# Kernel tuning notes

Measured on AMD Instinct MI355X. Metric: run time of the kernel, lower is better.

The kernel has to match this reference:

```python
import jax, jax.numpy as jnp
import numpy as np

D = 1024          # d_model
H = 16            # num_attention_heads
HD = D // H       # head_dim
WIN = 512         # attention_window (total)
W = WIN // 2      # one-sided window
S = 4096          # seq_len
B = 2             # batch
NEG = jnp.finfo(jnp.float32).min


def setup_inputs() -> dict:
    key = jax.random.key(0)
    ks = jax.random.split(key, 9)
    sc = 0.02
    return {
        "query": jax.random.normal(ks[0], (S, B, D), dtype=jnp.float32),
        "Wq": jax.random.normal(ks[1], (D, D), dtype=jnp.float32) * sc,
        "bq": jnp.zeros((D,), dtype=jnp.float32),
        "Wk": jax.random.normal(ks[2], (D, D), dtype=jnp.float32) * sc,
        "bk": jnp.zeros((D,), dtype=jnp.float32),
        "Wv": jax.random.normal(ks[3], (D, D), dtype=jnp.float32) * sc,
        "bv": jnp.zeros((D,), dtype=jnp.float32),
        "Wo": jax.random.normal(ks[4], (D, D), dtype=jnp.float32) * sc,
        "bo": jnp.zeros((D,), dtype=jnp.float32),
    }


def _heads(x):  # [B,S,D] -> [B,H,S,HD]
    b, s, _ = x.shape
    return x.reshape(b, s, H, HD).transpose(0, 2, 1, 3)


def reference(query, Wq, bq, Wk, bk, Wv, bv, Wo, bo):
    s, b, d = query.shape
    x = query.transpose(1, 0, 2)                       # [B,S,D]
    q = _heads(x @ Wq + bq) / jnp.sqrt(jnp.float32(HD))  # [B,H,S,HD]
    k = _heads(x @ Wk + bk)
    v = _heads(x @ Wv + bv)

    nc = s // W                                        # number of chunks
    # pad keys/values with one window of zeros on each side of seq axis
    kp = jnp.pad(k, ((0, 0), (0, 0), (W, W), (0, 0)))  # [B,H,S+2W,HD]
    vp = jnp.pad(v, ((0, 0), (0, 0), (W, W), (0, 0)))
    idx = jnp.arange(nc)[:, None] * W + jnp.arange(3 * W)[None, :]  # [nc,3W]
    kc = kp[:, :, idx]                                 # [B,H,nc,3W,HD]
    vc = vp[:, :, idx]
    qc = q.reshape(b, H, nc, W, HD)                    # [B,H,nc,W,HD]

    scores = jnp.einsum("bhcrd,bhckd->bhcrk", qc, kc)  # [B,H,nc,W,3W]

    r = jnp.arange(W)[:, None]                         # query offset in chunk
    kk = jnp.arange(3 * W)[None, :]
    band = (kk >= r) & (kk <= r + 2 * W)               # |kpos-qpos| <= W
    kpos = jnp.arange(nc)[:, None, None] * W + kk[None] - W   # [nc,1,3W] global key pos
    mask = band[None] & (kpos >= 0) & (kpos < s)       # [nc,W,3W]

    scores = jnp.where(mask[None, None], scores, NEG)
    probs = jax.nn.softmax(scores, axis=-1)
    out = jnp.einsum("bhcrk,bhckd->bhcrd", probs, vc)  # [B,H,nc,W,HD]
    out = out.reshape(b, H, s, HD).transpose(0, 2, 1, 3).reshape(b, s, d)
    out = out.transpose(1, 0, 2)                       # [S,B,D]
    return out @ Wo + bo
```

## Files before the change

kernel.cpp:

```cpp
#include <hip/hip_runtime.h>
#include <hip/hip_bf16.h>

#define SEQ 4096
#define BATCH 2
#define DMODEL 1024
#define NH 16
#define HDIM 64
#define NEGM (-1.0e30f)
#define NT 16

typedef __attribute__((ext_vector_type(8))) short bf16x8;
typedef __attribute__((ext_vector_type(8))) unsigned short us8;
typedef __attribute__((ext_vector_type(4))) unsigned short us4;
typedef __attribute__((ext_vector_type(4))) float f32x4;

__device__ __forceinline__ unsigned short f2bf(float f) {
    union { float f; unsigned u; } v; v.f = f;
    unsigned u = v.u;
    return (unsigned short)((u + 0x7fffu + ((u >> 16) & 1u)) >> 16);
}

#define GL16(g, l)                                                              \
    __builtin_amdgcn_global_load_lds(                                           \
        (const __attribute__((address_space(1))) unsigned int*)(g),             \
        (__attribute__((address_space(3))) unsigned int*)(l), 16, 0, 0)

__global__ __launch_bounds__(256) void transpose_all(const float* __restrict__ Wq,
                                                     const float* __restrict__ Wk,
                                                     const float* __restrict__ Wv,
                                                     const float* __restrict__ Wo,
                                                     unsigned short* __restrict__ wcat,
                                                     unsigned short* __restrict__ wot) {
    const int z = blockIdx.z;
    const float* W = (z == 0) ? Wq : (z == 1) ? Wk : (z == 2) ? Wv : Wo;
    unsigned short* Wt = (z == 3) ? wot : wcat + (size_t)z * 1024 * 1024;
    const float scale = (z == 0) ? 0.125f : 1.0f;
    __shared__ float tile[64][65];
    const int n0 = blockIdx.x * 64, k0 = blockIdx.y * 64;
    const int tx = threadIdx.x;
    for (int dy = threadIdx.y; dy < 64; dy += 4)
        tile[dy][tx] = W[(size_t)(k0 + dy) * DMODEL + n0 + tx];
    __syncthreads();
    for (int dy = threadIdx.y; dy < 64; dy += 4)
        Wt[(size_t)(n0 + dy) * DMODEL + k0 + tx] = f2bf(tile[tx][dy] * scale);
}

__global__ __launch_bounds__(256) void convert_x_bcat(const float* __restrict__ q,
                                                      unsigned short* __restrict__ xb,
                                                      const float* __restrict__ bq,
                                                      const float* __restrict__ bk,
                                                      const float* __restrict__ bv,
                                                      float* __restrict__ bcat) {
    const int bid = blockIdx.x;
    if (bid >= 8192) {
        int i = (bid - 8192) * 256 + threadIdx.x;
        float v;
        if (i < 1024) v = bq[i] * 0.125f;
        else if (i < 2048) v = bk[i - 1024];
        else v = bv[i - 2048];
        bcat[i] = v;
        return;
    }
    int t = bid * 256 + threadIdx.x;
    int d4 = (t & 255) * 4;
    int row = t >> 8;
    int b = row >> 12, s = row & (SEQ - 1);
    float4 v = *(const float4*)(q + ((size_t)s * BATCH + b) * DMODEL + d4);
    us4 o;
    o[0] = f2bf(v.x); o[1] = f2bf(v.y); o[2] = f2bf(v.z); o[3] = f2bf(v.w);
    *(us4*)(xb + (size_t)row * DMODEL + d4) = o;
}

__device__ __forceinline__ void store_qkv(float v0, float v1, float v2, float v3,
                                          int row0, int col, float bval,
                                          unsigned short* __restrict__ qb,
                                          unsigned short* __restrict__ kb,
                                          unsigned short* __restrict__ vtb) {
    const int proj = col >> 10;
    const int ch = col & 1023;
    const int h = ch >> 6, hd = ch & 63;
    float vv[4] = {v0, v1, v2, v3};
    if (proj == 2) {
        const int b = row0 >> 12, s = row0 & (SEQ - 1);
        us4 o;
#pragma unroll
        for (int r = 0; r < 4; ++r) o[r] = f2bf(vv[r] + bval);
        *(us4*)(vtb + ((size_t)(b * NH + h) * HDIM + hd) * SEQ + s) = o;
    } else {
        unsigned short* dst = (proj == 0) ? qb : kb;
#pragma unroll
        for (int r = 0; r < 4; ++r) {
            const int row = row0 + r;
            const int b = row >> 12, s = row & (SEQ - 1);
            dst[((size_t)(b * NH + h) * SEQ + s) * HDIM + hd] = f2bf(vv[r] + bval);
        }
    }
}

__global__ __launch_bounds__(512) void gemm192(const unsigned short* __restrict__ A,
                                               const unsigned short* __restrict__ Bt,
                                               const float* __restrict__ bias,
                                               unsigned short* __restrict__ qb,
                                               unsigned short* __restrict__ kb,
                                               unsigned short* __restrict__ vtb) {
    __shared__ __align__(16) unsigned short lds[57344];
    const int tid = threadIdx.x;
    const int lane = tid & 63, wid = tid >> 6;
    const int lr = lane & 15, lg = lane >> 4;
    const int wm = wid >> 2, wn = wid & 3;
    const int cpx = (int)gridDim.x >> 3;
    const int orig = ((int)blockIdx.x & 7) * cpx + ((int)blockIdx.x >> 3);
    const int m0 = (orig >> 4) * 256;
    const int n0 = (orig & 15) * 192;

    const int srow = wid * 8 + (lane >> 3);
    const int scol = ((lane & 7) ^ (lane >> 3)) << 3;

    f32x4 acc[8][3];
#pragma unroll
    for (int m = 0; m < 8; ++m)
#pragma unroll
        for (int n = 0; n < 3; ++n) {
            f32x4 z = {0.f, 0.f, 0.f, 0.f};
            acc[m][n] = z;
        }

    const unsigned short* gA = A + (size_t)(m0 + srow) * DMODEL + scol;
    const unsigned short* gB = Bt + (size_t)(n0 + srow) * DMODEL + scol;

#define STAGE192(kt, bsel)                                                       \
    do {                                                                         \
        const unsigned short* ga_ = gA + (kt) * 64;                              \
        unsigned short* la_ = &lds[(bsel) * 28672 + wid * 512];                  \
        _Pragma("unroll")                                                        \
        for (int r_ = 0; r_ < 4; ++r_)                                           \
            GL16(ga_ + (size_t)r_ * 64 * DMODEL, la_ + r_ * 4096);               \
        const unsigned short* gb_ = gB + (kt) * 64;                              \
        unsigned short* lb_ = &lds[(bsel) * 28672 + 16384 + wid * 512];          \
        _Pragma("unroll")                                                        \
        for (int r_ = 0; r_ < 3; ++r_)                                           \
            GL16(gb_ + (size_t)r_ * 64 * DMODEL, lb_ + r_ * 4096);               \
    } while (0)

    STAGE192(0, 0);
    asm volatile("s_waitcnt vmcnt(0)" ::: "memory");
    __builtin_amdgcn_s_barrier();
    asm volatile("" ::: "memory");

    const int swz = (lr & 7) << 3;
    for (int t = 0; t < NT; ++t) {
        if (t + 1 < NT) STAGE192(t + 1, (t + 1) & 1);
        const unsigned short* Ab = &lds[(t & 1) * 28672];
        const unsigned short* Bb = Ab + 16384;
#pragma unroll
        for (int ks = 0; ks < 2; ++ks) {
            const int kc = (ks * 32 + lg * 8) ^ swz;
            bf16x8 af[8], bfr[3];
#pragma unroll
            for (int fm = 0; fm < 8; ++fm)
                af[fm] = *(const bf16x8*)&Ab[(wm * 128 + fm * 16 + lr) * 64 + kc];
#pragma unroll
            for (int fn = 0; fn < 3; ++fn)
                bfr[fn] = *(const bf16x8*)&Bb[(wn * 48 + fn * 16 + lr) * 64 + kc];
            __builtin_amdgcn_s_setprio(1);
#pragma unroll
            for (int fm = 0; fm < 8; ++fm)
#pragma unroll
                for (int fn = 0; fn < 3; ++fn)
                    acc[fm][fn] = __builtin_amdgcn_mfma_f32_16x16x32_bf16(af[fm], bfr[fn], acc[fm][fn], 0, 0, 0);
            __builtin_amdgcn_s_setprio(0);
        }
        __builtin_amdgcn_sched_barrier(0);
        asm volatile("s_waitcnt lgkmcnt(0)" ::: "memory");
        asm volatile("s_waitcnt vmcnt(0)" ::: "memory");
        __builtin_amdgcn_s_barrier();
        asm volatile("" ::: "memory");
    }
#undef STAGE192

#pragma unroll
    for (int fn = 0; fn < 3; ++fn) {
        const int col = n0 + wn * 48 + fn * 16 + lr;
        const float bval = bias[col];
#pragma unroll
        for (int fm = 0; fm < 8; ++fm) {
            const int row0 = m0 + wm * 128 + fm * 16 + lg * 4;
            store_qkv(acc[fm][fn][0], acc[fm][fn][1], acc[fm][fn][2], acc[fm][fn][3],
                      row0, col, bval, qb, kb, vtb);
        }
    }
}

__global__ __launch_bounds__(512) void gemm256o(const unsigned short* __restrict__ A,
                                                const unsigned short* __restrict__ Bt,
                                                const float* __restrict__ bias,
                                                float* __restrict__ out) {
    __shared__ __align__(16) unsigned short lds[73728];
    const int tid = threadIdx.x;
    const int lane = tid & 63, wid = tid >> 6;
    const int lr = lane & 15, lg = lane >> 4;
    const int wm = wid >> 1, wn = wid & 1;
    const int cpx = (int)gridDim.x >> 3;
    const int orig = ((int)blockIdx.x & 7) * cpx + ((int)blockIdx.x >> 3);
    const int m0 = (orig >> 3) * 256;
    const int n0 = (orig & 7) * 128;

    const int srow = wid * 8 + (lane >> 3);
    const int scol = ((lane & 7) ^ (lane >> 3)) << 3;

    f32x4 acc[4][4];
#pragma unroll
    for (int m = 0; m < 4; ++m)
#pragma unroll
        for (int n = 0; n < 4; ++n) {
            f32x4 z = {0.f, 0.f, 0.f, 0.f};
            acc[m][n] = z;
        }

    const unsigned short* gA = A + (size_t)(m0 + srow) * DMODEL + scol;
    const unsigned short* gB = Bt + (size_t)(n0 + srow) * DMODEL + scol;

#define STAGE_A(kt, bsel)                                                        \
    do {                                                                         \
        const unsigned short* ga_ = gA + (kt) * 64;                              \
        unsigned short* la_ = &lds[(bsel) * 24576 + wid * 512];                  \
        _Pragma("unroll")                                                        \
        for (int r_ = 0; r_ < 4; ++r_)                                           \
            GL16(ga_ + (size_t)r_ * 64 * DMODEL, la_ + r_ * 4096);               \
    } while (0)
#define STAGE_B(kt, bsel)                                                        \
    do {                                                                         \
        const unsigned short* gb_ = gB + (kt) * 64;                              \
        unsigned short* lb_ = &lds[(bsel) * 24576 + 16384 + wid * 512];          \
        _Pragma("unroll")                                                        \
        for (int r_ = 0; r_ < 2; ++r_)                                           \
            GL16(gb_ + (size_t)r_ * 64 * DMODEL, lb_ + r_ * 4096);               \
    } while (0)

    STAGE_A(0, 0); STAGE_B(0, 0);
    STAGE_A(1, 1); STAGE_B(1, 1);
    asm volatile("s_waitcnt vmcnt(6)" ::: "memory");
    __builtin_amdgcn_s_barrier();
    asm volatile("" ::: "memory");

    const int swz = (lr & 7) << 3;
    int bs = 0;
    for (int t = 0; t < NT; ++t) {
        const int b2 = bs >= 1 ? bs - 1 : bs + 2;
        if (t + 2 < NT) { STAGE_A(t + 2, b2); STAGE_B(t + 2, b2); }
        const unsigned short* Ab = &lds[bs * 24576];
        const unsigned short* Bb = Ab + 16384;
#pragma unroll
        for (int ks = 0; ks < 2; ++ks) {
            const int kc = (ks * 32 + lg * 8) ^ swz;
            bf16x8 af[4], bfr[4];
#pragma unroll
            for (int fm = 0; fm < 4; ++fm)
                af[fm] = *(const bf16x8*)&Ab[(wm * 64 + fm * 16 + lr) * 64 + kc];
#pragma unroll
            for (int fn = 0; fn < 4; ++fn)
                bfr[fn] = *(const bf16x8*)&Bb[(wn * 64 + fn * 16 + lr) * 64 + kc];
            __builtin_amdgcn_s_setprio(1);
#pragma unroll
            for (int fm = 0; fm < 4; ++fm)
#pragma unroll
                for (int fn = 0; fn < 4; ++fn)
                    acc[fm][fn] = __builtin_amdgcn_mfma_f32_16x16x32_bf16(af[fm], bfr[fn], acc[fm][fn], 0, 0, 0);
            __builtin_amdgcn_s_setprio(0);
        }
        __builtin_amdgcn_sched_barrier(0);
        asm volatile("s_waitcnt lgkmcnt(0)" ::: "memory");
        if (t + 2 < NT)
            asm volatile("s_waitcnt vmcnt(6)" ::: "memory");
        else
            asm volatile("s_waitcnt vmcnt(0)" ::: "memory");
        __builtin_amdgcn_s_barrier();
        asm volatile("" ::: "memory");
        bs = bs < 2 ? bs + 1 : 0;
    }
#undef STAGE_A
#undef STAGE_B

#pragma unroll
    for (int fn = 0; fn < 4; ++fn) {
        const int col = n0 + wn * 64 + fn * 16 + lr;
        const float bval = bias[col];
#pragma unroll
        for (int fm = 0; fm < 4; ++fm) {
            const int row0 = m0 + wm * 64 + fm * 16 + lg * 4;
#pragma unroll
            for (int r = 0; r < 4; ++r) {
                const int row = row0 + r;
                const int b = row >> 12, s = row & (SEQ - 1);
                out[((size_t)s * BATCH + b) * DMODEL + col] = acc[fm][fn][r] + bval;
            }
        }
    }
}

__global__ __launch_bounds__(512) void attn_kernel(const unsigned short* __restrict__ qb,
                                                   const unsigned short* __restrict__ kb,
                                                   const unsigned short* __restrict__ vtb,
                                                   unsigned short* __restrict__ ao) {
    __shared__ __align__(16) unsigned short Ks[64][72];
    __shared__ __align__(16) unsigned short Vs[64][72];
    __shared__ __align__(16) unsigned short Ps[8][16][72];
    const int tid = threadIdx.x;
    const int lane = tid & 63, wid = tid >> 6;
    const int lr = lane & 15, lg = lane >> 4;
    const int blk = ((int)blockIdx.x & 7) * 128 + ((int)blockIdx.x >> 3);
    const int qc = blk & 31, h = (blk >> 5) & 15, b = blk >> 9;
    const int q0 = qc * 128;
    const unsigned short* Qh = qb + (size_t)(b * NH + h) * SEQ * HDIM;
    const unsigned short* Kh = kb + (size_t)(b * NH + h) * SEQ * HDIM;
    const unsigned short* Vh = vtb + (size_t)(b * NH + h) * HDIM * SEQ;
    const int qw = q0 + wid * 16;

    bf16x8 qf0 = *(const bf16x8*)(Qh + (size_t)(qw + lr) * HDIM + lg * 8);
    bf16x8 qf1 = *(const bf16x8*)(Qh + (size_t)(qw + lr) * HDIM + 32 + lg * 8);

    f32x4 oacc[4];
    float lsum[4];
#pragma unroll
    for (int n = 0; n < 4; ++n) {
        f32x4 z = {0.f, 0.f, 0.f, 0.f};
        oacc[n] = z;
    }
#pragma unroll
    for (int r = 0; r < 4; ++r) lsum[r] = 0.f;

    int lo = q0 - 256; if (lo < 0) lo = 0;
    int hi = q0 + 384; if (hi > SEQ) hi = SEQ;

    const int srow = tid >> 3, sseg = (tid & 7) * 8;

    us8 kpre = *(const us8*)(Kh + (size_t)(lo + srow) * HDIM + sseg);
    us8 vpre = *(const us8*)(Vh + (size_t)srow * SEQ + lo + sseg);

    for (int kt = lo; kt < hi; kt += 64) {
        __syncthreads();
        *(us8*)&Ks[srow][sseg] = kpre;
        *(us8*)&Vs[srow][sseg] = vpre;
        if (kt + 64 < hi) {
            kpre = *(const us8*)(Kh + (size_t)(kt + 64 + srow) * HDIM + sseg);
            vpre = *(const us8*)(Vh + (size_t)srow * SEQ + kt + 64 + sseg);
        }
        __builtin_amdgcn_sched_barrier(0);
        __syncthreads();

        f32x4 sf[4];
        __builtin_amdgcn_s_setprio(1);
#pragma unroll
        for (int n = 0; n < 4; ++n) {
            bf16x8 kf0 = *(const bf16x8*)&Ks[n * 16 + lr][lg * 8];
            bf16x8 kf1 = *(const bf16x8*)&Ks[n * 16 + lr][32 + lg * 8];
            f32x4 z = {0.f, 0.f, 0.f, 0.f};
            sf[n] = __builtin_amdgcn_mfma_f32_16x16x32_bf16(qf0, kf0, z, 0, 0, 0);
            sf[n] = __builtin_amdgcn_mfma_f32_16x16x32_bf16(qf1, kf1, sf[n], 0, 0, 0);
        }
        __builtin_amdgcn_s_setprio(0);
        const bool full = (kt >= qw - 241) && (kt + 63 <= qw + 256);
        if (!full) {
#pragma unroll
            for (int r = 0; r < 4; ++r) {
                const int qpos = qw + lg * 4 + r;
#pragma unroll
                for (int n = 0; n < 4; ++n) {
                    const int kpos = kt + n * 16 + lr;
                    if (kpos < qpos - 256 || kpos > qpos + 256) sf[n][r] = NEGM;
                }
            }
        }
#pragma unroll
        for (int n = 0; n < 4; ++n)
#pragma unroll
            for (int r = 0; r < 4; ++r) {
                const float p = __expf(sf[n][r]);
                lsum[r] += p;
                Ps[wid][lg * 4 + r][n * 16 + lr] = f2bf(p);
            }

        asm volatile("s_waitcnt lgkmcnt(0)" ::: "memory");
        __builtin_amdgcn_s_setprio(1);
#pragma unroll
        for (int ks = 0; ks < 2; ++ks) {
            bf16x8 pf = *(const bf16x8*)&Ps[wid][lr][ks * 32 + lg * 8];
#pragma unroll
            for (int n = 0; n < 4; ++n) {
                bf16x8 vf = *(const bf16x8*)&Vs[n * 16 + lr][ks * 32 + lg * 8];
                oacc[n] = __builtin_amdgcn_mfma_f32_16x16x32_bf16(pf, vf, oacc[n], 0, 0, 0);
            }
        }
        __builtin_amdgcn_s_setprio(0);
    }

#pragma unroll
    for (int d = 1; d < 16; d <<= 1)
#pragma unroll
        for (int r = 0; r < 4; ++r) lsum[r] += __shfl_xor(lsum[r], d, 64);

#pragma unroll
    for (int n = 0; n < 4; ++n)
#pragma unroll
        for (int r = 0; r < 4; ++r) {
            const int row = qw + lg * 4 + r;
            const float o = oacc[n][r] / lsum[r];
            ao[((size_t)b * SEQ + row) * DMODEL + h * HDIM + n * 16 + lr] = f2bf(o);
        }
}

extern "C" void kernel_launch(void* const* d_in, const int* in_sizes, int n_in,
                              void* d_out, int out_size, void* d_ws, size_t ws_size,
                              hipStream_t stream) {
    (void)in_sizes; (void)n_in; (void)out_size; (void)ws_size;
    const float* query = (const float*)d_in[0];
    const float* Wq = (const float*)d_in[1];
    const float* bq = (const float*)d_in[2];
    const float* Wk = (const float*)d_in[3];
    const float* bk = (const float*)d_in[4];
    const float* Wv = (const float*)d_in[5];
    const float* bv = (const float*)d_in[6];
    const float* Wo = (const float*)d_in[7];
    const float* bo = (const float*)d_in[8];
    float* out = (float*)d_out;

    char* ws = (char*)d_ws;
    unsigned short* xb   = (unsigned short*)ws;
    unsigned short* wcat = (unsigned short*)(ws + (16ull << 20));
    unsigned short* wot  = (unsigned short*)(ws + (22ull << 20));
    float*          bcat = (float*)(ws + (24ull << 20));
    unsigned short* qb   = (unsigned short*)(ws + (25ull << 20));
    unsigned short* kb   = (unsigned short*)(ws + (41ull << 20));
    unsigned short* vtb  = (unsigned short*)(ws + (57ull << 20));
    unsigned short* ao   = xb;

    transpose_all<<<dim3(16, 16, 4), dim3(64, 4), 0, stream>>>(Wq, Wk, Wv, Wo, wcat, wot);
    convert_x_bcat<<<8204, 256, 0, stream>>>(query, xb, bq, bk, bv, bcat);

    gemm192<<<512, 512, 0, stream>>>(xb, wcat, bcat, qb, kb, vtb);
    attn_kernel<<<1024, 512, 0, stream>>>(qb, kb, vtb, ao);
    gemm256o<<<256, 512, 0, stream>>>(ao, wot, bo, out);
}
```

Before: 149.0 us.

## Merge prep kernels, reshape QKV warp tiling, shrink output GEMM tiles

Fuses the weight transpose and the input/bias conversion into one launch, which saves a kernel launch. The QKV GEMM's 8 waves are regrouped from a 2x4 grid of 128x48 tiles to a 4x2 grid of 64x96 tiles, which changes the LDS fragment loads per MFMA. The output projection now uses 128x128 tiles with 256 threads and a single LDS buffer, so more blocks fit per CU for occupancy. In exchange it drops the triple-buffered load pipelining, so global loads no longer overlap with the MFMA work.

```diff
diff --git a/kernel.cpp b/kernel.cpp
--- a/kernel.cpp
+++ b/kernel.cpp
@@ -25,50 +25,50 @@
         (const __attribute__((address_space(1))) unsigned int*)(g),             \
         (__attribute__((address_space(3))) unsigned int*)(l), 16, 0, 0)
 
-__global__ __launch_bounds__(256) void transpose_all(const float* __restrict__ Wq,
-                                                     const float* __restrict__ Wk,
-                                                     const float* __restrict__ Wv,
-                                                     const float* __restrict__ Wo,
-                                                     unsigned short* __restrict__ wcat,
-                                                     unsigned short* __restrict__ wot) {
-    const int z = blockIdx.z;
-    const float* W = (z == 0) ? Wq : (z == 1) ? Wk : (z == 2) ? Wv : Wo;
-    unsigned short* Wt = (z == 3) ? wot : wcat + (size_t)z * 1024 * 1024;
-    const float scale = (z == 0) ? 0.125f : 1.0f;
+__global__ __launch_bounds__(256) void prep_all(const float* __restrict__ Wq,
+                                                const float* __restrict__ Wk,
+                                                const float* __restrict__ Wv,
+                                                const float* __restrict__ Wo,
+                                                const float* __restrict__ query,
+                                                const float* __restrict__ bq,
+                                                const float* __restrict__ bk,
+                                                const float* __restrict__ bv,
+                                                unsigned short* __restrict__ wcat,
+                                                unsigned short* __restrict__ wot,
+                                                unsigned short* __restrict__ xb,
+                                                float* __restrict__ bcat) {
     __shared__ float tile[64][65];
-    const int n0 = blockIdx.x * 64, k0 = blockIdx.y * 64;
-    const int tx = threadIdx.x;
-    for (int dy = threadIdx.y; dy < 64; dy += 4)
-        tile[dy][tx] = W[(size_t)(k0 + dy) * DMODEL + n0 + tx];
-    __syncthreads();
-    for (int dy = threadIdx.y; dy < 64; dy += 4)
-        Wt[(size_t)(n0 + dy) * DMODEL + k0 + tx] = f2bf(tile[tx][dy] * scale);
-}
-
-__global__ __launch_bounds__(256) void convert_x_bcat(const float* __restrict__ q,
-                                                      unsigned short* __restrict__ xb,
-                                                      const float* __restrict__ bq,
-                                                      const float* __restrict__ bk,
-                                                      const float* __restrict__ bv,
-                                                      float* __restrict__ bcat) {
     const int bid = blockIdx.x;
-    if (bid >= 8192) {
-        int i = (bid - 8192) * 256 + threadIdx.x;
+    const int tid = threadIdx.x;
+    if (bid < 1024) {
+        const int z = bid >> 8, by = (bid >> 4) & 15, bx = bid & 15;
+        const float* W = (z == 0) ? Wq : (z == 1) ? Wk : (z == 2) ? Wv : Wo;
+        unsigned short* Wt = (z == 3) ? wot : wcat + (size_t)z * 1024 * 1024;
+        const float scale = (z == 0) ? 0.125f : 1.0f;
+        const int n0 = bx * 64, k0 = by * 64;
+        const int tx = tid & 63, ty = tid >> 6;
+        for (int dy = ty; dy < 64; dy += 4)
+            tile[dy][tx] = W[(size_t)(k0 + dy) * DMODEL + n0 + tx];
+        __syncthreads();
+        for (int dy = ty; dy < 64; dy += 4)
+            Wt[(size_t)(n0 + dy) * DMODEL + k0 + tx] = f2bf(tile[tx][dy] * scale);
+    } else if (bid < 9216) {
+        int t = (bid - 1024) * 256 + tid;
+        int d4 = (t & 255) * 4;
+        int row = t >> 8;
+        int b = row >> 12, s = row & (SEQ - 1);
+        float4 v = *(const float4*)(query + ((size_t)s * BATCH + b) * DMODEL + d4);
+        us4 o;
+        o[0] = f2bf(v.x); o[1] = f2bf(v.y); o[2] = f2bf(v.z); o[3] = f2bf(v.w);
+        *(us4*)(xb + (size_t)row * DMODEL + d4) = o;
+    } else {
+        int i = (bid - 9216) * 256 + tid;
         float v;
         if (i < 1024) v = bq[i] * 0.125f;
         else if (i < 2048) v = bk[i - 1024];
         else v = bv[i - 2048];
         bcat[i] = v;
-        return;
-    }
-    int t = bid * 256 + threadIdx.x;
-    int d4 = (t & 255) * 4;
-    int row = t >> 8;
-    int b = row >> 12, s = row & (SEQ - 1);
-    float4 v = *(const float4*)(q + ((size_t)s * BATCH + b) * DMODEL + d4);
-    us4 o;
-    o[0] = f2bf(v.x); o[1] = f2bf(v.y); o[2] = f2bf(v.z); o[3] = f2bf(v.w);
-    *(us4*)(xb + (size_t)row * DMODEL + d4) = o;
+    }
 }
 
 __device__ __forceinline__ void store_qkv(float v0, float v1, float v2, float v3,
@@ -107,7 +107,7 @@
     const int tid = threadIdx.x;
     const int lane = tid & 63, wid = tid >> 6;
     const int lr = lane & 15, lg = lane >> 4;
-    const int wm = wid >> 2, wn = wid & 3;
+    const int wm = wid >> 1, wn = wid & 1;
     const int cpx = (int)gridDim.x >> 3;
     const int orig = ((int)blockIdx.x & 7) * cpx + ((int)blockIdx.x >> 3);
     const int m0 = (orig >> 4) * 256;
@@ -116,11 +116,11 @@
     const int srow = wid * 8 + (lane >> 3);
     const int scol = ((lane & 7) ^ (lane >> 3)) << 3;
 
-    f32x4 acc[8][3];
-#pragma unroll
-    for (int m = 0; m < 8; ++m)
-#pragma unroll
-        for (int n = 0; n < 3; ++n) {
+    f32x4 acc[4][6];
+#pragma unroll
+    for (int m = 0; m < 4; ++m)
+#pragma unroll
+        for (int n = 0; n < 6; ++n) {
             f32x4 z = {0.f, 0.f, 0.f, 0.f};
             acc[m][n] = z;
         }
@@ -155,18 +155,18 @@
 #pragma unroll
         for (int ks = 0; ks < 2; ++ks) {
             const int kc = (ks * 32 + lg * 8) ^ swz;
-            bf16x8 af[8], bfr[3];
-#pragma unroll
-            for (int fm = 0; fm < 8; ++fm)
-                af[fm] = *(const bf16x8*)&Ab[(wm * 128 + fm * 16 + lr) * 64 + kc];
-#pragma unroll
-            for (int fn = 0; fn < 3; ++fn)
-                bfr[fn] = *(const bf16x8*)&Bb[(wn * 48 + fn * 16 + lr) * 64 + kc];
+            bf16x8 af[4], bfr[6];
+#pragma unroll
+            for (int fm = 0; fm < 4; ++fm)
+                af[fm] = *(const bf16x8*)&Ab[(wm * 64 + fm * 16 + lr) * 64 + kc];
+#pragma unroll
+            for (int fn = 0; fn < 6; ++fn)
+                bfr[fn] = *(const bf16x8*)&Bb[(wn * 96 + fn * 16 + lr) * 64 + kc];
             __builtin_amdgcn_s_setprio(1);
 #pragma unroll
-            for (int fm = 0; fm < 8; ++fm)
-#pragma unroll
-                for (int fn = 0; fn < 3; ++fn)
+            for (int fm = 0; fm < 4; ++fm)
+#pragma unroll
+                for (int fn = 0; fn < 6; ++fn)
                     acc[fm][fn] = __builtin_amdgcn_mfma_f32_16x16x32_bf16(af[fm], bfr[fn], acc[fm][fn], 0, 0, 0);
             __builtin_amdgcn_s_setprio(0);
         }
@@ -179,30 +179,30 @@
 #undef STAGE192
 
 #pragma unroll
-    for (int fn = 0; fn < 3; ++fn) {
-        const int col = n0 + wn * 48 + fn * 16 + lr;
+    for (int fn = 0; fn < 6; ++fn) {
+        const int col = n0 + wn * 96 + fn * 16 + lr;
         const float bval = bias[col];
 #pragma unroll
-        for (int fm = 0; fm < 8; ++fm) {
-            const int row0 = m0 + wm * 128 + fm * 16 + lg * 4;
+        for (int fm = 0; fm < 4; ++fm) {
+            const int row0 = m0 + wm * 64 + fm * 16 + lg * 4;
             store_qkv(acc[fm][fn][0], acc[fm][fn][1], acc[fm][fn][2], acc[fm][fn][3],
                       row0, col, bval, qb, kb, vtb);
         }
     }
 }
 
-__global__ __launch_bounds__(512) void gemm256o(const unsigned short* __restrict__ A,
-                                                const unsigned short* __restrict__ Bt,
-                                                const float* __restrict__ bias,
-                                                float* __restrict__ out) {
-    __shared__ __align__(16) unsigned short lds[73728];
+__global__ __launch_bounds__(256, 4) void gemm128o(const unsigned short* __restrict__ A,
+                                                   const unsigned short* __restrict__ Bt,
+                                                   const float* __restrict__ bias,
+                                                   float* __restrict__ out) {
+    __shared__ __align__(16) unsigned short lds[16384];
     const int tid = threadIdx.x;
     const int lane = tid & 63, wid = tid >> 6;
     const int lr = lane & 15, lg = lane >> 4;
     const int wm = wid >> 1, wn = wid & 1;
     const int cpx = (int)gridDim.x >> 3;
     const int orig = ((int)blockIdx.x & 7) * cpx + ((int)blockIdx.x >> 3);
-    const int m0 = (orig >> 3) * 256;
+    const int m0 = (orig >> 3) * 128;
     const int n0 = (orig & 7) * 128;
 
     const int srow = wid * 8 + (lane >> 3);
@@ -219,47 +219,34 @@
 
     const unsigned short* gA = A + (size_t)(m0 + srow) * DMODEL + scol;
     const unsigned short* gB = Bt + (size_t)(n0 + srow) * DMODEL + scol;
-
-#define STAGE_A(kt, bsel)                                                        \
-    do {                                                                         \
-        const unsigned short* ga_ = gA + (kt) * 64;                              \
-        unsigned short* la_ = &lds[(bsel) * 24576 + wid * 512];                  \
-        _Pragma("unroll")                                                        \
-        for (int r_ = 0; r_ < 4; ++r_)                                           \
-            GL16(ga_ + (size_t)r_ * 64 * DMODEL, la_ + r_ * 4096);               \
-    } while (0)
-#define STAGE_B(kt, bsel)                                                        \
-    do {                                                                         \
-        const unsigned short* gb_ = gB + (kt) * 64;                              \
-        unsigned short* lb_ = &lds[(bsel) * 24576 + 16384 + wid * 512];          \
-        _Pragma("unroll")                                                        \
-        for (int r_ = 0; r_ < 2; ++r_)                                           \
-            GL16(gb_ + (size_t)r_ * 64 * DMODEL, lb_ + r_ * 4096);               \
-    } while (0)
-
-    STAGE_A(0, 0); STAGE_B(0, 0);
-    STAGE_A(1, 1); STAGE_B(1, 1);
-    asm volatile("s_waitcnt vmcnt(6)" ::: "memory");
-    __builtin_amdgcn_s_barrier();
-    asm volatile("" ::: "memory");
-
     const int swz = (lr & 7) << 3;
-    int bs = 0;
+
     for (int t = 0; t < NT; ++t) {
-        const int b2 = bs >= 1 ? bs - 1 : bs + 2;
-        if (t + 2 < NT) { STAGE_A(t + 2, b2); STAGE_B(t + 2, b2); }
-        const unsigned short* Ab = &lds[bs * 24576];
-        const unsigned short* Bb = Ab + 16384;
+        {
+            const unsigned short* ga_ = gA + t * 64;
+            unsigned short* la_ = &lds[wid * 512];
+#pragma unroll
+            for (int r_ = 0; r_ < 4; ++r_)
+                GL16(ga_ + (size_t)r_ * 32 * DMODEL, la_ + r_ * 2048);
+            const unsigned short* gb_ = gB + t * 64;
+            unsigned short* lb_ = &lds[8192 + wid * 512];
+#pragma unroll
+            for (int r_ = 0; r_ < 4; ++r_)
+                GL16(gb_ + (size_t)r_ * 32 * DMODEL, lb_ + r_ * 2048);
+        }
+        asm volatile("s_waitcnt vmcnt(0)" ::: "memory");
+        __builtin_amdgcn_s_barrier();
+        asm volatile("" ::: "memory");
 #pragma unroll
         for (int ks = 0; ks < 2; ++ks) {
             const int kc = (ks * 32 + lg * 8) ^ swz;
             bf16x8 af[4], bfr[4];
 #pragma unroll
             for (int fm = 0; fm < 4; ++fm)
-                af[fm] = *(const bf16x8*)&Ab[(wm * 64 + fm * 16 + lr) * 64 + kc];
+                af[fm] = *(const bf16x8*)&lds[(wm * 64 + fm * 16 + lr) * 64 + kc];
 #pragma unroll
             for (int fn = 0; fn < 4; ++fn)
-                bfr[fn] = *(const bf16x8*)&Bb[(wn * 64 + fn * 16 + lr) * 64 + kc];
+                bfr[fn] = *(const bf16x8*)&lds[8192 + (wn * 64 + fn * 16 + lr) * 64 + kc];
             __builtin_amdgcn_s_setprio(1);
 #pragma unroll
             for (int fm = 0; fm < 4; ++fm)
@@ -270,16 +257,9 @@
         }
         __builtin_amdgcn_sched_barrier(0);
         asm volatile("s_waitcnt lgkmcnt(0)" ::: "memory");
-        if (t + 2 < NT)
-            asm volatile("s_waitcnt vmcnt(6)" ::: "memory");
-        else
-            asm volatile("s_waitcnt vmcnt(0)" ::: "memory");
         __builtin_amdgcn_s_barrier();
         asm volatile("" ::: "memory");
-        bs = bs < 2 ? bs + 1 : 0;
-    }
-#undef STAGE_A
-#undef STAGE_B
+    }
 
 #pragma unroll
     for (int fn = 0; fn < 4; ++fn) {
@@ -434,10 +414,9 @@
     unsigned short* vtb  = (unsigned short*)(ws + (57ull << 20));
     unsigned short* ao   = xb;
 
-    transpose_all<<<dim3(16, 16, 4), dim3(64, 4), 0, stream>>>(Wq, Wk, Wv, Wo, wcat, wot);
-    convert_x_bcat<<<8204, 256, 0, stream>>>(query, xb, bq, bk, bv, bcat);
-
+    prep_all<<<9228, 256, 0, stream>>>(Wq, Wk, Wv, Wo, query, bq, bk, bv,
+                                       wcat, wot, xb, bcat);
     gemm192<<<512, 512, 0, stream>>>(xb, wcat, bcat, qb, kb, vtb);
     attn_kernel<<<1024, 512, 0, stream>>>(qb, kb, vtb, ao);
-    gemm256o<<<256, 512, 0, stream>>>(ao, wot, bo, out);
-}
+    gemm128o<<<512, 256, 0, stream>>>(ao, wot, bo, out);
+}
```

Result: faster. 140.5 us (median of 3 runs) (-5.7%).
